# Kernel tuning notes

Hardware: AMD Instinct MI355X
Metric: run time of the kernel (lower is better)

Reference implementation:

```python
import jax, jax.numpy as jnp
import numpy as np

B = 512        # batch of parallel sequences
TM1 = 64       # T-1 recurrence steps
BELIEF = 2048  # GRU / deterministic belief size
STATE = 256    # stochastic state size
ACTION = 64
HIDDEN = 2048
EMB = 1024     # embedding_size['fusion']
MIN_STD = 0.1


def setup_inputs() -> dict:
    key = jax.random.key(0)
    ks = jax.random.split(key, 16)
    w = lambda k, shape: jax.random.normal(k, shape, dtype=jnp.float32) * 0.02
    return {
        "prev_state": jax.random.normal(ks[0], (B, STATE), dtype=jnp.float32),
        "actions": jax.random.normal(ks[1], (TM1, B, ACTION), dtype=jnp.float32),
        "prev_belief": jax.random.normal(ks[2], (B, BELIEF), dtype=jnp.float32),
        "obs_emb": jax.random.normal(ks[3], (TM1, B, EMB), dtype=jnp.float32),
        "nonterminals": jnp.ones((TM1, B, 1), dtype=jnp.float32),
        # fc_embed_state_action
        "W_embed": w(ks[4], (STATE + ACTION, BELIEF)),
        "b_embed": jnp.zeros((BELIEF,), jnp.float32),
        # GRUCell (input-to-hidden / hidden-to-hidden, gate order r,z,n as torch)
        "Wi": w(ks[5], (BELIEF, 3 * BELIEF)),
        "bi": jnp.zeros((3 * BELIEF,), jnp.float32),
        "Wh": w(ks[6], (BELIEF, 3 * BELIEF)),
        "bh": jnp.zeros((3 * BELIEF,), jnp.float32),
        # stochastic_state_model (prior): h -> hidden -> 2*state
        "W1": w(ks[7], (BELIEF, HIDDEN)),
        "b1": jnp.zeros((HIDDEN,), jnp.float32),
        "W2": w(ks[8], (HIDDEN, 2 * STATE)),
        "b2": jnp.zeros((2 * STATE,), jnp.float32),
        # obs_encoder (posterior): cat(h, obs_emb) -> hidden -> 2*state
        "W1p": w(ks[9], (BELIEF + EMB, HIDDEN)),
        "b1p": jnp.zeros((HIDDEN,), jnp.float32),
        "W2p": w(ks[10], (HIDDEN, 2 * STATE)),
        "b2p": jnp.zeros((2 * STATE,), jnp.float32),
        # reparameterized-sampling noise (rsample = loc + scale * eps)
        "eps_prior": jax.random.normal(ks[11], (TM1, B, STATE), dtype=jnp.float32),
        "eps_post": jax.random.normal(ks[12], (TM1, B, STATE), dtype=jnp.float32),
    }


def reference(prev_state, actions, prev_belief, obs_emb, nonterminals,
              W_embed, b_embed, Wi, bi, Wh, bh,
              W1, b1, W2, b2, W1p, b1p, W2p, b2p,
              eps_prior, eps_post):
    def step(carry, xs):
        belief, post_state = carry
        a, obs, nt, ep, eq = xs
        s = post_state * nt                                   # [B, S]
        hidden = jax.nn.relu(jnp.concatenate([s, a], axis=1) @ W_embed + b_embed)
        # torch.nn.GRUCell math (gate order r, z, n)
        gi = hidden @ Wi + bi
        gh = belief @ Wh + bh
        i_r, i_z, i_n = jnp.split(gi, 3, axis=1)
        h_r, h_z, h_n = jnp.split(gh, 3, axis=1)
        r = jax.nn.sigmoid(i_r + h_r)
        z = jax.nn.sigmoid(i_z + h_z)
        n = jnp.tanh(i_n + r * h_n)
        new_belief = (1.0 - z) * n + z * belief               # [B, H]
        # prior stochastic state model
        hp = jax.nn.relu(new_belief @ W1 + b1)
        loc_p, raw_p = jnp.split(hp @ W2 + b2, 2, axis=1)
        scale_p = jax.nn.softplus(raw_p) + MIN_STD
        prior_state = loc_p + scale_p * ep                    # rsample
        # posterior from obs embedding
        hq = jax.nn.relu(jnp.concatenate([new_belief, obs], axis=1) @ W1p + b1p)
        loc_q, raw_q = jnp.split(hq @ W2p + b2p, 2, axis=1)
        scale_q = jax.nn.softplus(raw_q) + MIN_STD
        post_new = loc_q + scale_q * eq                       # rsample
        ys = (new_belief, prior_state, loc_p, scale_p, post_new, loc_q, scale_q)
        return (new_belief, post_new), ys

    _, ys = jax.lax.scan(step, (prev_belief, prev_state),
                         (actions, obs_emb, nonterminals, eps_prior, eps_post))
    # (beliefs, prior_states, prior_means, prior_std_devs,
    #  posterior_states, posterior_means, posterior_std_devs), each [T-1, B, ...]
    return ys
```

## Files before the change

kernel.cpp:

```cpp
#include <hip/hip_runtime.h>
#include <hip/hip_bf16.h>
#include <cstdint>

typedef __hip_bfloat16 bf16;
typedef __attribute__((ext_vector_type(8))) short bf16x8v;
typedef __attribute__((ext_vector_type(4))) float f32x4;

#define TM1 64
#define BATCH 512
#define BELIEF 2048
#define STATE 256
#define ACTION 64
#define HIDDEN 2048
#define EMB 1024

#define OUT_BEL  ((size_t)0)
#define OUT_PST  ((size_t)67108864)
#define OUT_PMU  ((size_t)75497472)
#define OUT_PSD  ((size_t)83886080)
#define OUT_QST  ((size_t)92274688)
#define OUT_QMU  ((size_t)100663296)
#define OUT_QSD  ((size_t)109051904)

__device__ __forceinline__ void gload_lds16(const bf16* g, bf16* l) {
  __builtin_amdgcn_global_load_lds(
      (const __attribute__((address_space(1))) unsigned int*)g,
      (__attribute__((address_space(3))) unsigned int*)l, 16, 0, 0);
}

template<int BM, int BN, int MODE>
__global__ __launch_bounds__(256)
void gemm_bt(const bf16* __restrict__ A0, const bf16* __restrict__ A1,
             const bf16* __restrict__ B0, const bf16* __restrict__ B1,
             const float* __restrict__ bias0, const float* __restrict__ bias1,
             void* __restrict__ C0, void* __restrict__ C1,
             int M, int N, int K)
{
  constexpr int BK = 64;
  constexpr int WMt = BM / 2, WNt = BN / 2;
  constexpr int MR = WMt / 16, NR = WNt / 16;

  const bf16* A = A0; const bf16* B = B0; const float* bias = bias0; void* Cv = C0;
  if (blockIdx.z) { A = A1; B = B1; bias = bias1; Cv = C1; }

  const int m0 = blockIdx.y * BM;
  const int n0 = blockIdx.x * BN;

  __shared__ __align__(16) bf16 sA[BM * BK];
  __shared__ __align__(16) bf16 sB[BN * BK];

  const int tid = threadIdx.x;
  const int lane = tid & 63;
  const int wid = tid >> 6;
  const int wm = wid >> 1, wn = wid & 1;
  const int lr = lane & 15;
  const int ko = (lane >> 4) * 8;

  f32x4 acc[MR][NR] = {};

  for (int k0 = 0; k0 < K; k0 += BK) {
    __syncthreads();
    #pragma unroll
    for (int i = 0; i < BM * 8 / 256; ++i) {
      int c = i * 256 + tid;
      int row = c >> 3, koct = c & 7;
      gload_lds16(A + (size_t)(m0 + row) * K + k0 + koct * 8, &sA[c * 8]);
    }
    #pragma unroll
    for (int i = 0; i < BN * 8 / 256; ++i) {
      int c = i * 256 + tid;
      int row = c >> 3, koct = c & 7;
      gload_lds16(B + (size_t)(n0 + row) * K + k0 + koct * 8, &sB[c * 8]);
    }
    __syncthreads();

    #pragma unroll
    for (int kk = 0; kk < 2; ++kk) {
      bf16x8v af[MR], bfv[NR];
      #pragma unroll
      for (int m = 0; m < MR; ++m)
        af[m] = *(const bf16x8v*)&sA[(wm * WMt + m * 16 + lr) * BK + kk * 32 + ko];
      #pragma unroll
      for (int n = 0; n < NR; ++n)
        bfv[n] = *(const bf16x8v*)&sB[(wn * WNt + n * 16 + lr) * BK + kk * 32 + ko];
      #pragma unroll
      for (int m = 0; m < MR; ++m)
        #pragma unroll
        for (int n = 0; n < NR; ++n)
          acc[m][n] = __builtin_amdgcn_mfma_f32_16x16x32_bf16(af[m], bfv[n], acc[m][n], 0, 0, 0);
    }
  }

  const int r0 = (lane >> 4) * 4;
  #pragma unroll
  for (int m = 0; m < MR; ++m) {
    #pragma unroll
    for (int n = 0; n < NR; ++n) {
      int gc = n0 + wn * WNt + n * 16 + lr;
      float bv = bias[gc];
      #pragma unroll
      for (int r = 0; r < 4; ++r) {
        int gr = m0 + wm * WMt + m * 16 + r0 + r;
        float v = acc[m][n][r] + bv;
        if (MODE == 1) {
          ((bf16*)Cv)[(size_t)gr * N + gc] = __float2bfloat16(v > 0.f ? v : 0.f);
        } else {
          ((float*)Cv)[(size_t)gr * N + gc] = v;
        }
      }
    }
  }
}

__global__ void transpose_cvt(const float* __restrict__ src, bf16* __restrict__ dst,
                              int K, int N)
{
  __shared__ float t[32][33];
  int n0 = blockIdx.x * 32, k0 = blockIdx.y * 32;
  int tx = threadIdx.x, ty = threadIdx.y;
  #pragma unroll
  for (int i = 0; i < 32; i += 8)
    t[ty + i][tx] = src[(size_t)(k0 + ty + i) * N + n0 + tx];
  __syncthreads();
  #pragma unroll
  for (int i = 0; i < 32; i += 8)
    dst[(size_t)(n0 + ty + i) * K + k0 + tx] = __float2bfloat16(t[tx][ty + i]);
}

__global__ void init_belief(const float* __restrict__ prev_belief,
                            float* __restrict__ bf32, bf16* __restrict__ bb16)
{
  int i = blockIdx.x * 256 + threadIdx.x;
  float v = prev_belief[i];
  bf32[i] = v;
  bb16[i] = __float2bfloat16(v);
}

__global__ void xcat0_kernel(const float* __restrict__ prev_state,
                             const float* __restrict__ nt0,
                             const float* __restrict__ act0,
                             bf16* __restrict__ xcat)
{
  int idx = blockIdx.x * 256 + threadIdx.x;
  if (idx >= BATCH * (STATE + ACTION)) return;
  int b = idx / (STATE + ACTION);
  int c = idx - b * (STATE + ACTION);
  float v;
  if (c < STATE) v = prev_state[b * STATE + c] * nt0[b];
  else           v = act0[b * ACTION + (c - STATE)];
  xcat[idx] = __float2bfloat16(v);
}

__device__ __forceinline__ float sigmoidf_(float x) { return 1.f / (1.f + __expf(-x)); }

__global__ void gru_ew(const float* __restrict__ gi, const float* __restrict__ gh,
                       float* __restrict__ belief_f32, bf16* __restrict__ belief_b16,
                       float* __restrict__ out_bel_t, bf16* __restrict__ hqcat,
                       const float* __restrict__ obs_t)
{
  int idx = blockIdx.x * 256 + threadIdx.x;
  int b = idx >> 11;
  int c = idx & 2047;
  size_t base = (size_t)b * 3 * BELIEF;
  float ir = gi[base + c], iz = gi[base + BELIEF + c], in_ = gi[base + 2 * BELIEF + c];
  float hr = gh[base + c], hz = gh[base + BELIEF + c], hn  = gh[base + 2 * BELIEF + c];
  float r = sigmoidf_(ir + hr);
  float z = sigmoidf_(iz + hz);
  float n = tanhf(in_ + r * hn);
  float nb = (1.f - z) * n + z * belief_f32[idx];
  belief_f32[idx] = nb;
  bf16 v = __float2bfloat16(nb);
  belief_b16[idx] = v;
  out_bel_t[idx] = nb;
  hqcat[(size_t)b * (BELIEF + EMB) + c] = v;
  if (c < EMB)
    hqcat[(size_t)b * (BELIEF + EMB) + BELIEF + c] = __float2bfloat16(obs_t[(size_t)b * EMB + c]);
}

__global__ void post_ew(const float* __restrict__ yq, const float* __restrict__ eps,
                        float* __restrict__ o_mu, float* __restrict__ o_sd,
                        float* __restrict__ o_st,
                        const float* __restrict__ nt_next, const float* __restrict__ act_next,
                        bf16* __restrict__ xcat, int make_xcat)
{
  int idx = blockIdx.x * 256 + threadIdx.x;
  int b = idx >> 8;
  int j = idx & 255;
  float loc = yq[(size_t)b * 512 + j];
  float raw = yq[(size_t)b * 512 + 256 + j];
  float sp = (raw > 20.f) ? raw : log1pf(__expf(raw));
  float scale = sp + 0.1f;
  float st = loc + scale * eps[idx];
  o_mu[idx] = loc;
  o_sd[idx] = scale;
  o_st[idx] = st;
  if (make_xcat) {
    xcat[(size_t)b * (STATE + ACTION) + j] = __float2bfloat16(st * nt_next[b]);
    if (j < ACTION)
      xcat[(size_t)b * (STATE + ACTION) + STATE + j] =
          __float2bfloat16(act_next[(size_t)b * ACTION + j]);
  }
}

__global__ void cvt_f32_bf16(const float* __restrict__ src, bf16* __restrict__ dst, int n)
{
  int i = blockIdx.x * 256 + threadIdx.x;
  if (i < n) dst[i] = __float2bfloat16(src[i]);
}

__global__ void prior_ew(const float* __restrict__ yp, const float* __restrict__ eps,
                         float* __restrict__ o_mu, float* __restrict__ o_sd,
                         float* __restrict__ o_st)
{
  int idx = blockIdx.x * 256 + threadIdx.x;
  int r = idx >> 8;
  int j = idx & 255;
  float loc = yp[(size_t)r * 512 + j];
  float raw = yp[(size_t)r * 512 + 256 + j];
  float sp = (raw > 20.f) ? raw : log1pf(__expf(raw));
  float scale = sp + 0.1f;
  o_mu[idx] = loc;
  o_sd[idx] = scale;
  o_st[idx] = loc + scale * eps[idx];
}

extern "C" void kernel_launch(void* const* d_in, const int* in_sizes, int n_in,
                              void* d_out, int out_size, void* d_ws, size_t ws_size,
                              hipStream_t stream)
{
  (void)in_sizes; (void)n_in; (void)out_size; (void)ws_size;
  const float* prev_state = (const float*)d_in[0];
  const float* actions    = (const float*)d_in[1];
  const float* prev_belief= (const float*)d_in[2];
  const float* obs_emb    = (const float*)d_in[3];
  const float* nonterm    = (const float*)d_in[4];
  const float* W_embed    = (const float*)d_in[5];
  const float* b_embed    = (const float*)d_in[6];
  const float* Wi         = (const float*)d_in[7];
  const float* bi         = (const float*)d_in[8];
  const float* Wh         = (const float*)d_in[9];
  const float* bh         = (const float*)d_in[10];
  const float* W1         = (const float*)d_in[11];
  const float* b1         = (const float*)d_in[12];
  const float* W2         = (const float*)d_in[13];
  const float* b2         = (const float*)d_in[14];
  const float* W1p        = (const float*)d_in[15];
  const float* b1p        = (const float*)d_in[16];
  const float* W2p        = (const float*)d_in[17];
  const float* b2p        = (const float*)d_in[18];
  const float* eps_p      = (const float*)d_in[19];
  const float* eps_q      = (const float*)d_in[20];
  float* out = (float*)d_out;

  char* ws = (char*)d_ws;
  size_t off = 0;
  auto alloc = [&](size_t bytes) -> char* {
    char* p = ws + off;
    off = (off + bytes + 255) & ~(size_t)255;
    return p;
  };
  bf16* WembT = (bf16*)alloc((size_t)2048 * 320 * 2);
  bf16* WiT   = (bf16*)alloc((size_t)6144 * 2048 * 2);
  bf16* WhT   = (bf16*)alloc((size_t)6144 * 2048 * 2);
  bf16* W1T   = (bf16*)alloc((size_t)2048 * 2048 * 2);
  bf16* W2T   = (bf16*)alloc((size_t)512 * 2048 * 2);
  bf16* W1pT  = (bf16*)alloc((size_t)2048 * 3072 * 2);
  bf16* W2pT  = (bf16*)alloc((size_t)512 * 2048 * 2);
  float* belief_f32 = (float*)alloc((size_t)BATCH * BELIEF * 4);
  bf16*  belief_b16 = (bf16*)alloc((size_t)BATCH * BELIEF * 2);
  bf16*  xcat       = (bf16*)alloc((size_t)BATCH * (STATE + ACTION) * 2);
  bf16*  hidden     = (bf16*)alloc((size_t)BATCH * BELIEF * 2);
  float* gi         = (float*)alloc((size_t)BATCH * 3 * BELIEF * 4);
  float* gh         = (float*)alloc((size_t)BATCH * 3 * BELIEF * 4);
  bf16*  hqcat      = (bf16*)alloc((size_t)BATCH * (BELIEF + EMB) * 2);
  bf16*  hq         = (bf16*)alloc((size_t)BATCH * HIDDEN * 2);
  float* yq         = (float*)alloc((size_t)BATCH * 512 * 4);
  bf16*  belA       = (bf16*)alloc((size_t)4096 * BELIEF * 2);
  bf16*  hp         = (bf16*)alloc((size_t)4096 * HIDDEN * 2);
  float* yp         = (float*)alloc((size_t)4096 * 512 * 4);

  dim3 tb(32, 8);
  transpose_cvt<<<dim3(2048/32, 320/32),  tb, 0, stream>>>(W_embed, WembT, 320, 2048);
  transpose_cvt<<<dim3(6144/32, 2048/32), tb, 0, stream>>>(Wi, WiT, 2048, 6144);
  transpose_cvt<<<dim3(6144/32, 2048/32), tb, 0, stream>>>(Wh, WhT, 2048, 6144);
  transpose_cvt<<<dim3(2048/32, 2048/32), tb, 0, stream>>>(W1, W1T, 2048, 2048);
  transpose_cvt<<<dim3(512/32, 2048/32),  tb, 0, stream>>>(W2, W2T, 2048, 512);
  transpose_cvt<<<dim3(2048/32, 3072/32), tb, 0, stream>>>(W1p, W1pT, 3072, 2048);
  transpose_cvt<<<dim3(512/32, 2048/32),  tb, 0, stream>>>(W2p, W2pT, 2048, 512);

  init_belief<<<(BATCH * BELIEF) / 256, 256, 0, stream>>>(prev_belief, belief_f32, belief_b16);
  xcat0_kernel<<<(BATCH * (STATE + ACTION) + 255) / 256, 256, 0, stream>>>(
      prev_state, nonterm, actions, xcat);

  for (int t = 0; t < TM1; ++t) {
    gemm_bt<128, 128, 1><<<dim3(16, 4, 1), 256, 0, stream>>>(
        xcat, nullptr, WembT, nullptr, b_embed, nullptr, hidden, nullptr,
        512, 2048, 320);
    gemm_bt<128, 128, 0><<<dim3(48, 4, 2), 256, 0, stream>>>(
        hidden, belief_b16, WiT, WhT, bi, bh, gi, gh,
        512, 6144, 2048);
    gru_ew<<<(BATCH * BELIEF) / 256, 256, 0, stream>>>(
        gi, gh, belief_f32, belief_b16,
        out + OUT_BEL + (size_t)t * BATCH * BELIEF,
        hqcat, obs_emb + (size_t)t * BATCH * EMB);
    gemm_bt<64, 128, 1><<<dim3(16, 8, 1), 256, 0, stream>>>(
        hqcat, nullptr, W1pT, nullptr, b1p, nullptr, hq, nullptr,
        512, 2048, 3072);
    gemm_bt<64, 64, 0><<<dim3(8, 8, 1), 256, 0, stream>>>(
        hq, nullptr, W2pT, nullptr, b2p, nullptr, yq, nullptr,
        512, 512, 2048);
    post_ew<<<(BATCH * STATE) / 256, 256, 0, stream>>>(
        yq, eps_q + (size_t)t * BATCH * STATE,
        out + OUT_QMU + (size_t)t * BATCH * STATE,
        out + OUT_QSD + (size_t)t * BATCH * STATE,
        out + OUT_QST + (size_t)t * BATCH * STATE,
        nonterm + (size_t)(t + 1) * BATCH,
        actions + (size_t)(t + 1) * BATCH * ACTION,
        xcat, (t < TM1 - 1) ? 1 : 0);
  }

  for (int c = 0; c < 8; ++c) {
    const float* belsrc = out + OUT_BEL + (size_t)c * 4096 * BELIEF;
    cvt_f32_bf16<<<(4096 * BELIEF) / 256, 256, 0, stream>>>(belsrc, belA, 4096 * BELIEF);
    gemm_bt<128, 128, 1><<<dim3(16, 32, 1), 256, 0, stream>>>(
        belA, nullptr, W1T, nullptr, b1, nullptr, hp, nullptr,
        4096, 2048, 2048);
    gemm_bt<128, 64, 0><<<dim3(8, 32, 1), 256, 0, stream>>>(
        hp, nullptr, W2T, nullptr, b2, nullptr, yp, nullptr,
        4096, 512, 2048);
    prior_ew<<<(4096 * 256) / 256, 256, 0, stream>>>(
        yp, eps_p + (size_t)c * 4096 * STATE,
        out + OUT_PMU + (size_t)c * 4096 * STATE,
        out + OUT_PSD + (size_t)c * 4096 * STATE,
        out + OUT_PST + (size_t)c * 4096 * STATE);
  }
}
```

Baseline: 10.31 ms.

## Overlap prior GEMMs with recurrence via multi-descriptor GEMM launches and split-K posterior head

Replaces the per-step GEMM kernel with a multi-descriptor GEMM that packs several independent GEMMs into one launch. It moves the hidden-state GEMM for the next step next to the posterior MLP, and interleaves the batched prior-model GEMMs (run on a ring buffer of bf16 beliefs every 8 steps) with the small per-step recurrence GEMMs to fill idle CUs. The posterior output GEMM becomes a 4-way split-K whose last-arriving tile reduces partial sums through atomic counters and runs the softplus/sampling epilogue, which removes the separate post_ew launch. Other changes are an XCD-aware block remap, a vectorized GRU elementwise kernel, and removal of the f32-to-bf16 conversion pass. The risks are atomic counter reset ordering, extra partial-sum traffic, and larger, less regular launches.

```diff
diff --git a/kernel.cpp b/kernel.cpp
--- a/kernel.cpp
+++ b/kernel.cpp
@@ -28,26 +28,46 @@
       (__attribute__((address_space(3))) unsigned int*)l, 16, 0, 0);
 }
 
-template<int BM, int BN, int MODE>
+__device__ __forceinline__ unsigned short bfb(float f) {
+  bf16 h = __float2bfloat16(f);
+  return *reinterpret_cast<unsigned short*>(&h);
+}
+
+struct GDesc {
+  const bf16* A; const bf16* B; const float* bias; void* C;
+  int M, N, K, ksplit, mode, nb;
+};
+struct PostArgs {
+  const float* eps; float* o_mu; float* o_sd; float* o_st;
+  const float* nt_next; const float* act_next; bf16* xcat;
+  unsigned* counters; int make_xcat;
+};
+
+template<int BM, int BN>
 __global__ __launch_bounds__(256)
-void gemm_bt(const bf16* __restrict__ A0, const bf16* __restrict__ A1,
-             const bf16* __restrict__ B0, const bf16* __restrict__ B1,
-             const float* __restrict__ bias0, const float* __restrict__ bias1,
-             void* __restrict__ C0, void* __restrict__ C1,
-             int M, int N, int K)
-{
-  constexpr int BK = 64;
-  constexpr int WMt = BM / 2, WNt = BN / 2;
-  constexpr int MR = WMt / 16, NR = WNt / 16;
-
-  const bf16* A = A0; const bf16* B = B0; const float* bias = bias0; void* Cv = C0;
-  if (blockIdx.z) { A = A1; B = B1; bias = bias1; Cv = C1; }
-
-  const int m0 = blockIdx.y * BM;
-  const int n0 = blockIdx.x * BN;
-
-  __shared__ __align__(16) bf16 sA[BM * BK];
-  __shared__ __align__(16) bf16 sB[BN * BK];
+void gemm_multi(GDesc d0, GDesc d1, GDesc d2, PostArgs pa)
+{
+  const int nwg = gridDim.x;
+  const int orig = blockIdx.x;
+  const int q8 = nwg >> 3, r8 = nwg & 7;
+  const int xcd = orig & 7, oo = orig >> 3;
+  int bid = (xcd < r8 ? xcd * (q8 + 1) : r8 * (q8 + 1) + (xcd - r8) * q8) + oo;
+
+  GDesc d = d0;
+  if (bid >= d.nb) { bid -= d.nb; d = d1; if (bid >= d.nb) { bid -= d.nb; d = d2; } }
+
+  const int nm = d.M / BM;
+  const int per = nm * (d.N / BN);
+  const int ks  = bid / per;
+  const int rem = bid - ks * per;
+  const int mb  = rem % nm;
+  const int nbk = rem / nm;
+  const int m0 = mb * BM, n0 = nbk * BN;
+  const int Kc = d.K / d.ksplit;
+  const int kbeg = ks * Kc, kend = kbeg + Kc;
+
+  __shared__ __align__(16) bf16 sA[BM * 64];
+  __shared__ __align__(16) bf16 sB[BN * 64];
 
   const int tid = threadIdx.x;
   const int lane = tid & 63;
@@ -55,22 +75,27 @@
   const int wm = wid >> 1, wn = wid & 1;
   const int lr = lane & 15;
   const int ko = (lane >> 4) * 8;
+  constexpr int WMt = BM / 2, WNt = BN / 2;
+  constexpr int MR = WMt / 16, NR = WNt / 16;
 
   f32x4 acc[MR][NR] = {};
 
-  for (int k0 = 0; k0 < K; k0 += BK) {
+  const bf16* Abase = d.A + (size_t)m0 * d.K;
+  const bf16* Bbase = d.B + (size_t)n0 * d.K;
+
+  for (int k0 = kbeg; k0 < kend; k0 += 64) {
     __syncthreads();
     #pragma unroll
-    for (int i = 0; i < BM * 8 / 256; ++i) {
+    for (int i = 0; i < BM / 32; ++i) {
       int c = i * 256 + tid;
-      int row = c >> 3, koct = c & 7;
-      gload_lds16(A + (size_t)(m0 + row) * K + k0 + koct * 8, &sA[c * 8]);
+      int row = c >> 3, kc = (c & 7) * 8;
+      gload_lds16(Abase + (size_t)row * d.K + k0 + kc, &sA[c * 8]);
     }
     #pragma unroll
-    for (int i = 0; i < BN * 8 / 256; ++i) {
+    for (int i = 0; i < BN / 32; ++i) {
       int c = i * 256 + tid;
-      int row = c >> 3, koct = c & 7;
-      gload_lds16(B + (size_t)(n0 + row) * K + k0 + koct * 8, &sB[c * 8]);
+      int row = c >> 3, kc = (c & 7) * 8;
+      gload_lds16(Bbase + (size_t)row * d.K + k0 + kc, &sB[c * 8]);
     }
     __syncthreads();
 
@@ -79,10 +104,10 @@
       bf16x8v af[MR], bfv[NR];
       #pragma unroll
       for (int m = 0; m < MR; ++m)
-        af[m] = *(const bf16x8v*)&sA[(wm * WMt + m * 16 + lr) * BK + kk * 32 + ko];
+        af[m] = *(const bf16x8v*)&sA[(wm * WMt + m * 16 + lr) * 64 + kk * 32 + ko];
       #pragma unroll
       for (int n = 0; n < NR; ++n)
-        bfv[n] = *(const bf16x8v*)&sB[(wn * WNt + n * 16 + lr) * BK + kk * 32 + ko];
+        bfv[n] = *(const bf16x8v*)&sB[(wn * WNt + n * 16 + lr) * 64 + kk * 32 + ko];
       #pragma unroll
       for (int m = 0; m < MR; ++m)
         #pragma unroll
@@ -92,20 +117,71 @@
   }
 
   const int r0 = (lane >> 4) * 4;
-  #pragma unroll
-  for (int m = 0; m < MR; ++m) {
+  if (d.mode != 3) {
     #pragma unroll
-    for (int n = 0; n < NR; ++n) {
-      int gc = n0 + wn * WNt + n * 16 + lr;
-      float bv = bias[gc];
+    for (int m = 0; m < MR; ++m) {
       #pragma unroll
-      for (int r = 0; r < 4; ++r) {
-        int gr = m0 + wm * WMt + m * 16 + r0 + r;
-        float v = acc[m][n][r] + bv;
-        if (MODE == 1) {
-          ((bf16*)Cv)[(size_t)gr * N + gc] = __float2bfloat16(v > 0.f ? v : 0.f);
-        } else {
-          ((float*)Cv)[(size_t)gr * N + gc] = v;
+      for (int n = 0; n < NR; ++n) {
+        int gc = n0 + wn * WNt + n * 16 + lr;
+        float bv = d.bias[gc];
+        #pragma unroll
+        for (int r = 0; r < 4; ++r) {
+          int gr = m0 + wm * WMt + m * 16 + r0 + r;
+          float v = acc[m][n][r] + bv;
+          if (d.mode == 1)
+            ((bf16*)d.C)[(size_t)gr * d.N + gc] = __float2bfloat16(v > 0.f ? v : 0.f);
+          else
+            ((float*)d.C)[(size_t)gr * d.N + gc] = v;
+        }
+      }
+    }
+  } else {
+    float* P = (float*)d.C + (size_t)ks * d.M * d.N;
+    #pragma unroll
+    for (int m = 0; m < MR; ++m)
+      #pragma unroll
+      for (int n = 0; n < NR; ++n) {
+        int gc = n0 + wn * WNt + n * 16 + lr;
+        #pragma unroll
+        for (int r = 0; r < 4; ++r) {
+          int gr = m0 + wm * WMt + m * 16 + r0 + r;
+          P[(size_t)gr * d.N + gc] = acc[m][n][r];
+        }
+      }
+    __threadfence();
+    __syncthreads();
+    __shared__ unsigned tic;
+    const int pair = mb * 4 + (nbk & 3);
+    if (tid == 0) tic = atomicAdd(&pa.counters[pair], 1u);
+    __syncthreads();
+    if (tic == 7) {
+      __threadfence();
+      const int nl = nbk & 3;
+      const float* Y = (const float*)d.C;
+      for (int e = tid; e < 64 * 64; e += 256) {
+        int rr = e >> 6, cc = e & 63;
+        int b = m0 + rr;
+        int j = nl * 64 + cc;
+        float loc = d.bias[j], raw = d.bias[256 + j];
+        #pragma unroll
+        for (int k2 = 0; k2 < 4; ++k2) {
+          loc += Y[(size_t)k2 * 262144 + (size_t)b * 512 + j];
+          raw += Y[(size_t)k2 * 262144 + (size_t)b * 512 + 256 + j];
+        }
+        float sp = (raw > 20.f) ? raw : log1pf(__expf(raw));
+        float scale = sp + 0.1f;
+        float st = loc + scale * pa.eps[b * 256 + j];
+        pa.o_mu[b * 256 + j] = loc;
+        pa.o_sd[b * 256 + j] = scale;
+        pa.o_st[b * 256 + j] = st;
+        if (pa.make_xcat)
+          pa.xcat[b * 320 + j] = __float2bfloat16(st * pa.nt_next[b]);
+      }
+      if (pa.make_xcat && nl == 0) {
+        for (int e = tid; e < 64 * 64; e += 256) {
+          int rr = e >> 6, cc = e & 63;
+          int b = m0 + rr;
+          pa.xcat[b * 320 + 256 + cc] = __float2bfloat16(pa.act_next[b * 64 + cc]);
         }
       }
     }
@@ -153,59 +229,48 @@
 
 __device__ __forceinline__ float sigmoidf_(float x) { return 1.f / (1.f + __expf(-x)); }
 
-__global__ void gru_ew(const float* __restrict__ gi, const float* __restrict__ gh,
-                       float* __restrict__ belief_f32, bf16* __restrict__ belief_b16,
-                       float* __restrict__ out_bel_t, bf16* __restrict__ hqcat,
-                       const float* __restrict__ obs_t)
-{
-  int idx = blockIdx.x * 256 + threadIdx.x;
-  int b = idx >> 11;
-  int c = idx & 2047;
-  size_t base = (size_t)b * 3 * BELIEF;
-  float ir = gi[base + c], iz = gi[base + BELIEF + c], in_ = gi[base + 2 * BELIEF + c];
-  float hr = gh[base + c], hz = gh[base + BELIEF + c], hn  = gh[base + 2 * BELIEF + c];
+__device__ __forceinline__ float gru1(float ir, float hr, float iz, float hz,
+                                      float in_, float hn, float bo)
+{
   float r = sigmoidf_(ir + hr);
   float z = sigmoidf_(iz + hz);
   float n = tanhf(in_ + r * hn);
-  float nb = (1.f - z) * n + z * belief_f32[idx];
-  belief_f32[idx] = nb;
-  bf16 v = __float2bfloat16(nb);
-  belief_b16[idx] = v;
-  out_bel_t[idx] = nb;
-  hqcat[(size_t)b * (BELIEF + EMB) + c] = v;
-  if (c < EMB)
-    hqcat[(size_t)b * (BELIEF + EMB) + BELIEF + c] = __float2bfloat16(obs_t[(size_t)b * EMB + c]);
-}
-
-__global__ void post_ew(const float* __restrict__ yq, const float* __restrict__ eps,
-                        float* __restrict__ o_mu, float* __restrict__ o_sd,
-                        float* __restrict__ o_st,
-                        const float* __restrict__ nt_next, const float* __restrict__ act_next,
-                        bf16* __restrict__ xcat, int make_xcat)
-{
-  int idx = blockIdx.x * 256 + threadIdx.x;
-  int b = idx >> 8;
-  int j = idx & 255;
-  float loc = yq[(size_t)b * 512 + j];
-  float raw = yq[(size_t)b * 512 + 256 + j];
-  float sp = (raw > 20.f) ? raw : log1pf(__expf(raw));
-  float scale = sp + 0.1f;
-  float st = loc + scale * eps[idx];
-  o_mu[idx] = loc;
-  o_sd[idx] = scale;
-  o_st[idx] = st;
-  if (make_xcat) {
-    xcat[(size_t)b * (STATE + ACTION) + j] = __float2bfloat16(st * nt_next[b]);
-    if (j < ACTION)
-      xcat[(size_t)b * (STATE + ACTION) + STATE + j] =
-          __float2bfloat16(act_next[(size_t)b * ACTION + j]);
-  }
-}
-
-__global__ void cvt_f32_bf16(const float* __restrict__ src, bf16* __restrict__ dst, int n)
-{
-  int i = blockIdx.x * 256 + threadIdx.x;
-  if (i < n) dst[i] = __float2bfloat16(src[i]);
+  return (1.f - z) * n + z * bo;
+}
+
+__global__ void gru_ew(const float* __restrict__ gi, const float* __restrict__ gh,
+                       float* __restrict__ belief, float* __restrict__ out_bel,
+                       bf16* __restrict__ roll_slot, bf16* __restrict__ hqcat,
+                       const float* __restrict__ obs_t, unsigned* __restrict__ counters)
+{
+  int tid = threadIdx.x;
+  if (blockIdx.x == 0 && tid < 32) counters[tid] = 0;
+  int i = blockIdx.x * 256 + tid;
+  int b = i >> 9;
+  int c = (i & 511) * 4;
+  size_t gb = (size_t)b * 6144;
+  float4 ir = *(const float4*)&gi[gb + c];
+  float4 iz = *(const float4*)&gi[gb + 2048 + c];
+  float4 in_ = *(const float4*)&gi[gb + 4096 + c];
+  float4 hr = *(const float4*)&gh[gb + c];
+  float4 hz = *(const float4*)&gh[gb + 2048 + c];
+  float4 hn = *(const float4*)&gh[gb + 4096 + c];
+  float4 bo = *(const float4*)&belief[(size_t)b * 2048 + c];
+  float4 nb;
+  nb.x = gru1(ir.x, hr.x, iz.x, hz.x, in_.x, hn.x, bo.x);
+  nb.y = gru1(ir.y, hr.y, iz.y, hz.y, in_.y, hn.y, bo.y);
+  nb.z = gru1(ir.z, hr.z, iz.z, hz.z, in_.z, hn.z, bo.z);
+  nb.w = gru1(ir.w, hr.w, iz.w, hz.w, in_.w, hn.w, bo.w);
+  *(float4*)&belief[(size_t)b * 2048 + c] = nb;
+  *(float4*)&out_bel[(size_t)b * 2048 + c] = nb;
+  ushort4 u; u.x = bfb(nb.x); u.y = bfb(nb.y); u.z = bfb(nb.z); u.w = bfb(nb.w);
+  *(ushort4*)&roll_slot[(size_t)b * 2048 + c] = u;
+  *(ushort4*)&hqcat[(size_t)b * 3072 + c] = u;
+  if ((i & 511) < 256) {
+    float4 ov = *(const float4*)&obs_t[(size_t)b * 1024 + c];
+    ushort4 uo; uo.x = bfb(ov.x); uo.y = bfb(ov.y); uo.z = bfb(ov.z); uo.w = bfb(ov.w);
+    *(ushort4*)&hqcat[(size_t)b * 3072 + 2048 + c] = uo;
+  }
 }
 
 __global__ void prior_ew(const float* __restrict__ yp, const float* __restrict__ eps,
@@ -267,17 +332,29 @@
   bf16* W1pT  = (bf16*)alloc((size_t)2048 * 3072 * 2);
   bf16* W2pT  = (bf16*)alloc((size_t)512 * 2048 * 2);
   float* belief_f32 = (float*)alloc((size_t)BATCH * BELIEF * 4);
-  bf16*  belief_b16 = (bf16*)alloc((size_t)BATCH * BELIEF * 2);
-  bf16*  xcat       = (bf16*)alloc((size_t)BATCH * (STATE + ACTION) * 2);
+  bf16*  bel_init   = (bf16*)alloc((size_t)BATCH * BELIEF * 2);
+  bf16*  roll       = (bf16*)alloc((size_t)8 * BATCH * BELIEF * 2);
+  bf16*  xcat       = (bf16*)alloc((size_t)BATCH * 320 * 2);
   bf16*  hidden     = (bf16*)alloc((size_t)BATCH * BELIEF * 2);
   float* gi         = (float*)alloc((size_t)BATCH * 3 * BELIEF * 4);
   float* gh         = (float*)alloc((size_t)BATCH * 3 * BELIEF * 4);
-  bf16*  hqcat      = (bf16*)alloc((size_t)BATCH * (BELIEF + EMB) * 2);
+  bf16*  hqcat      = (bf16*)alloc((size_t)BATCH * 3072 * 2);
   bf16*  hq         = (bf16*)alloc((size_t)BATCH * HIDDEN * 2);
-  float* yq         = (float*)alloc((size_t)BATCH * 512 * 4);
-  bf16*  belA       = (bf16*)alloc((size_t)4096 * BELIEF * 2);
+  float* yqp        = (float*)alloc((size_t)4 * 512 * 512 * 4);
   bf16*  hp         = (bf16*)alloc((size_t)4096 * HIDDEN * 2);
   float* yp         = (float*)alloc((size_t)4096 * 512 * 4);
+  unsigned* counters= (unsigned*)alloc(32 * 4);
+
+  auto mk = [](const bf16* A, const bf16* B, const float* bias, void* C,
+               int M, int N, int K, int ksplit, int mode, int BM, int BN) {
+    GDesc g; g.A = A; g.B = B; g.bias = bias; g.C = C;
+    g.M = M; g.N = N; g.K = K; g.ksplit = ksplit; g.mode = mode;
+    g.nb = (M / BM) * (N / BN) * ksplit;
+    return g;
+  };
+  GDesc dz128 = mk(nullptr, nullptr, nullptr, nullptr, 128, 128, 64, 1, 0, 128, 128); dz128.nb = 0;
+  GDesc dz64  = mk(nullptr, nullptr, nullptr, nullptr, 64, 64, 64, 1, 0, 64, 64);     dz64.nb = 0;
+  PostArgs pz{}; pz.counters = counters;
 
   dim3 tb(32, 8);
   transpose_cvt<<<dim3(2048/32, 320/32),  tb, 0, stream>>>(W_embed, WembT, 320, 2048);
@@ -288,50 +365,72 @@
   transpose_cvt<<<dim3(2048/32, 3072/32), tb, 0, stream>>>(W1p, W1pT, 3072, 2048);
   transpose_cvt<<<dim3(512/32, 2048/32),  tb, 0, stream>>>(W2p, W2pT, 2048, 512);
 
-  init_belief<<<(BATCH * BELIEF) / 256, 256, 0, stream>>>(prev_belief, belief_f32, belief_b16);
-  xcat0_kernel<<<(BATCH * (STATE + ACTION) + 255) / 256, 256, 0, stream>>>(
-      prev_state, nonterm, actions, xcat);
+  init_belief<<<(BATCH * BELIEF) / 256, 256, 0, stream>>>(prev_belief, belief_f32, bel_init);
+  xcat0_kernel<<<(BATCH * 320 + 255) / 256, 256, 0, stream>>>(prev_state, nonterm, actions, xcat);
+
+  {
+    GDesc e = mk(xcat, WembT, b_embed, hidden, 512, 2048, 320, 1, 1, 64, 64);
+    gemm_multi<64,64><<<e.nb, 256, 0, stream>>>(e, dz64, dz64, pz);
+  }
+  {
+    GDesc g = mk(bel_init, WhT, bh, gh, 512, 6144, 2048, 1, 0, 128, 128);
+    gemm_multi<128,128><<<g.nb, 256, 0, stream>>>(g, dz128, dz128, pz);
+  }
 
   for (int t = 0; t < TM1; ++t) {
-    gemm_bt<128, 128, 1><<<dim3(16, 4, 1), 256, 0, stream>>>(
-        xcat, nullptr, WembT, nullptr, b_embed, nullptr, hidden, nullptr,
-        512, 2048, 320);
-    gemm_bt<128, 128, 0><<<dim3(48, 4, 2), 256, 0, stream>>>(
-        hidden, belief_b16, WiT, WhT, bi, bh, gi, gh,
-        512, 6144, 2048);
-    gru_ew<<<(BATCH * BELIEF) / 256, 256, 0, stream>>>(
-        gi, gh, belief_f32, belief_b16,
+    const bool pr = (t > 0 && (t & 7) == 0);
+    GDesc a0 = mk(hidden, WiT, bi, gi, 512, 6144, 2048, 1, 0, 128, 128);
+    GDesc a1 = pr ? mk(roll, W1T, b1, hp, 4096, 2048, 2048, 1, 1, 128, 128) : dz128;
+    gemm_multi<128,128><<<a0.nb + a1.nb, 256, 0, stream>>>(a0, a1, dz128, pz);
+
+    gru_ew<<<1024, 256, 0, stream>>>(
+        gi, gh, belief_f32,
         out + OUT_BEL + (size_t)t * BATCH * BELIEF,
-        hqcat, obs_emb + (size_t)t * BATCH * EMB);
-    gemm_bt<64, 128, 1><<<dim3(16, 8, 1), 256, 0, stream>>>(
-        hqcat, nullptr, W1pT, nullptr, b1p, nullptr, hq, nullptr,
-        512, 2048, 3072);
-    gemm_bt<64, 64, 0><<<dim3(8, 8, 1), 256, 0, stream>>>(
-        hq, nullptr, W2pT, nullptr, b2p, nullptr, yq, nullptr,
-        512, 512, 2048);
-    post_ew<<<(BATCH * STATE) / 256, 256, 0, stream>>>(
-        yq, eps_q + (size_t)t * BATCH * STATE,
-        out + OUT_QMU + (size_t)t * BATCH * STATE,
-        out + OUT_QSD + (size_t)t * BATCH * STATE,
-        out + OUT_QST + (size_t)t * BATCH * STATE,
-        nonterm + (size_t)(t + 1) * BATCH,
-        actions + (size_t)(t + 1) * BATCH * ACTION,
-        xcat, (t < TM1 - 1) ? 1 : 0);
-  }
-
-  for (int c = 0; c < 8; ++c) {
-    const float* belsrc = out + OUT_BEL + (size_t)c * 4096 * BELIEF;
-    cvt_f32_bf16<<<(4096 * BELIEF) / 256, 256, 0, stream>>>(belsrc, belA, 4096 * BELIEF);
-    gemm_bt<128, 128, 1><<<dim3(16, 32, 1), 256, 0, stream>>>(
-        belA, nullptr, W1T, nullptr, b1, nullptr, hp, nullptr,
-        4096, 2048, 2048);
-    gemm_bt<128, 64, 0><<<dim3(8, 32, 1), 256, 0, stream>>>(
-        hp, nullptr, W2T, nullptr, b2, nullptr, yp, nullptr,
-        4096, 512, 2048);
-    prior_ew<<<(4096 * 256) / 256, 256, 0, stream>>>(
-        yp, eps_p + (size_t)c * 4096 * STATE,
-        out + OUT_PMU + (size_t)c * 4096 * STATE,
-        out + OUT_PSD + (size_t)c * 4096 * STATE,
-        out + OUT_PST + (size_t)c * 4096 * STATE);
-  }
-}
+        roll + (size_t)(t & 7) * BATCH * BELIEF,
+        hqcat, obs_emb + (size_t)t * BATCH * EMB, counters);
+
+    GDesc b0 = mk(hqcat, W1pT, b1p, hq, 512, 2048, 3072, 1, 1, 128, 128);
+    GDesc b1d = (t < TM1 - 1)
+        ? mk(roll + (size_t)(t & 7) * BATCH * BELIEF, WhT, bh, gh, 512, 6144, 2048, 1, 0, 128, 128)
+        : dz128;
+    gemm_multi<128,128><<<b0.nb + b1d.nb, 256, 0, stream>>>(b0, b1d, dz128, pz);
+
+    GDesc c0 = mk(hq, W2pT, b2p, yqp, 512, 512, 2048, 4, 3, 64, 64);
+    GDesc c1 = pr ? mk(hp, W2T, b2, yp, 4096, 512, 2048, 1, 0, 64, 64) : dz64;
+    PostArgs pa;
+    pa.eps = eps_q + (size_t)t * BATCH * STATE;
+    pa.o_mu = out + OUT_QMU + (size_t)t * BATCH * STATE;
+    pa.o_sd = out + OUT_QSD + (size_t)t * BATCH * STATE;
+    pa.o_st = out + OUT_QST + (size_t)t * BATCH * STATE;
+    int tn = (t < TM1 - 1) ? t + 1 : t;
+    pa.nt_next  = nonterm + (size_t)tn * BATCH;
+    pa.act_next = actions + (size_t)tn * BATCH * ACTION;
+    pa.xcat = xcat; pa.counters = counters; pa.make_xcat = (t < TM1 - 1) ? 1 : 0;
+    gemm_multi<64,64><<<c0.nb + c1.nb, 256, 0, stream>>>(c0, c1, dz64, pa);
+
+    if (pr) {
+      int c = (t >> 3) - 1;
+      prior_ew<<<4096, 256, 0, stream>>>(
+          yp, eps_p + (size_t)c * 4096 * STATE,
+          out + OUT_PMU + (size_t)c * 4096 * STATE,
+          out + OUT_PSD + (size_t)c * 4096 * STATE,
+          out + OUT_PST + (size_t)c * 4096 * STATE);
+    }
+    if (t < TM1 - 1) {
+      GDesc e = mk(xcat, WembT, b_embed, hidden, 512, 2048, 320, 1, 1, 64, 64);
+      gemm_multi<64,64><<<e.nb, 256, 0, stream>>>(e, dz64, dz64, pz);
+    }
+  }
+
+  {
+    GDesc p1 = mk(roll, W1T, b1, hp, 4096, 2048, 2048, 1, 1, 128, 128);
+    gemm_multi<128,128><<<p1.nb, 256, 0, stream>>>(p1, dz128, dz128, pz);
+    GDesc p2 = mk(hp, W2T, b2, yp, 4096, 512, 2048, 1, 0, 64, 64);
+    gemm_multi<64,64><<<p2.nb, 256, 0, stream>>>(p2, dz64, dz64, pz);
+    prior_ew<<<4096, 256, 0, stream>>>(
+        yp, eps_p + (size_t)7 * 4096 * STATE,
+        out + OUT_PMU + (size_t)7 * 4096 * STATE,
+        out + OUT_PSD + (size_t)7 * 4096 * STATE,
+        out + OUT_PST + (size_t)7 * 4096 * STATE);
+  }
+}
```

Result: slower. 13.42 ms (+30.2%).
